# Kernel tuning notes

Measured on AMD Instinct MI355X. Metric: run time of the kernel, lower is better.

Reference implementation:

```python
import jax, jax.numpy as jnp
import numpy as np

N_NODES = 40000
N_EDGES = 320000
N_GRAPHS = 64
IN_DIM = 128
HID4 = 256   # hidden_dim * 4
OUT_DIM = 128
LN_EPS = 1e-5


def setup_inputs() -> dict:
    key = jax.random.key(0)
    ks = jax.random.split(key, 12)
    x = jax.random.normal(ks[0], (N_NODES, IN_DIM), dtype=jnp.float32)
    w = jax.random.uniform(ks[1], (N_EDGES, 4), dtype=jnp.float32)
    src = jax.random.randint(ks[2], (N_EDGES,), 0, N_NODES, dtype=jnp.int32)
    dst = jax.random.randint(ks[3], (N_EDGES,), 0, N_NODES, dtype=jnp.int32)
    graph_ids = jnp.sort(jax.random.randint(ks[4], (N_NODES,), 0, N_GRAPHS, dtype=jnp.int32))
    # parameters (no biases on GraphConv / fc1 linear)
    W1 = jax.random.normal(ks[5], (IN_DIM, HID4), dtype=jnp.float32) / np.sqrt(IN_DIM)
    fc1_W = jax.random.normal(ks[6], (IN_DIM, HID4), dtype=jnp.float32) / np.sqrt(IN_DIM)
    ln_gamma = jnp.ones((HID4,), dtype=jnp.float32)
    ln_beta = jnp.zeros((HID4,), dtype=jnp.float32)
    W2 = jax.random.normal(ks[7], (2 * HID4, HID4), dtype=jnp.float32) / np.sqrt(2 * HID4)
    W3 = jax.random.normal(ks[8], (HID4, OUT_DIM), dtype=jnp.float32) / np.sqrt(HID4)
    return {"x": x, "w": w, "W1": W1, "fc1_W": fc1_W, "ln_gamma": ln_gamma,
            "ln_beta": ln_beta, "W2": W2, "W3": W3,
            "src": src, "dst": dst, "graph_ids": graph_ids}


def _graph_conv(feat, src, dst, ew, W, out_inv_sqrt, in_inv_sqrt):
    # DGL GraphConv, norm='both', bias=False, with scalar edge_weight:
    # h = D_out^{-1/2} x ; m_e = w_e * h[src] ; agg = scatter_add(m, dst) ;
    # out = (D_in^{-1/2} agg) @ W
    h = feat * out_inv_sqrt[:, None]
    m = h[src] * ew[:, None]                       # [E, D] messages
    agg = jax.ops.segment_sum(m, dst, num_segments=N_NODES)
    return (agg * in_inv_sqrt[:, None]) @ W


def reference(x, w, W1, fc1_W, ln_gamma, ln_beta, W2, W3, src, dst, graph_ids):
    # unweighted degree normalization (DGL uses structural degrees, clamp(min=1))
    ones_e = jnp.ones((N_EDGES,), dtype=x.dtype)
    out_deg = jnp.maximum(jax.ops.segment_sum(ones_e, src, num_segments=N_NODES), 1.0)
    in_deg = jnp.maximum(jax.ops.segment_sum(ones_e, dst, num_segments=N_NODES), 1.0)
    out_inv = out_deg ** -0.5
    in_inv = in_deg ** -0.5

    ew = jnp.max(w, axis=1)                        # [E]

    x1 = jax.nn.relu(_graph_conv(x, src, dst, ew, W1, out_inv, in_inv))

    # fc1: Linear(no bias) -> LayerNorm(affine) -> ReLU
    f1 = x @ fc1_W
    mu = jnp.mean(f1, axis=-1, keepdims=True)
    var = jnp.mean((f1 - mu) ** 2, axis=-1, keepdims=True)
    f1 = (f1 - mu) * jax.lax.rsqrt(var + LN_EPS) * ln_gamma + ln_beta
    f1 = jax.nn.relu(f1)

    x1f1 = jnp.concatenate([x1, f1], axis=1)       # [N, 512]
    x2 = jax.nn.relu(_graph_conv(x1f1, src, dst, ew, W2, out_inv, in_inv))
    x3 = jax.nn.relu(_graph_conv(x2, src, dst, ew, W3, out_inv, in_inv))

    # dgl.sum_nodes over batched graph, then row-wise L2 normalize
    readout = jax.ops.segment_sum(x3, graph_ids, num_segments=N_GRAPHS)  # [G, OUT_DIM]
    norm = jnp.maximum(jnp.linalg.norm(readout, axis=1, keepdims=True), 1e-12)
    return readout / norm
```

## Files before the change

kernel.cpp:

```cpp
#include <hip/hip_runtime.h>

#define N_NODES 40000
#define M_PAD   40064
#define N_EDGES 320000
#define N_GRAPHS 64
#define IN_DIM 128
#define HID4 256
#define OUT_DIM 128
#define LN_EPS 1e-5f

typedef short  s16x8  __attribute__((ext_vector_type(8)));
typedef __bf16 bf16x8 __attribute__((ext_vector_type(8)));
typedef float  f32x4  __attribute__((ext_vector_type(4)));

__device__ __forceinline__ unsigned short f2b(float f) {
    unsigned int u = __builtin_bit_cast(unsigned int, f);
    u += 0x7fffu + ((u >> 16) & 1u);
    return (unsigned short)(u >> 16);
}
__device__ __forceinline__ float b2f(unsigned short h) {
    unsigned int u = (unsigned int)h << 16;
    return __builtin_bit_cast(float, u);
}
__device__ __forceinline__ float lo2f(unsigned int u) { return b2f((unsigned short)u); }
__device__ __forceinline__ float hi2f(unsigned int u) { return b2f((unsigned short)(u >> 16)); }
__device__ __forceinline__ unsigned int packb(float x, float y) {
    return (unsigned int)f2b(x) | ((unsigned int)f2b(y) << 16);
}

__device__ __forceinline__ void gll16(const unsigned short* g, short* lds_base) {
    __builtin_amdgcn_global_load_lds(
        (const __attribute__((address_space(1))) unsigned int*)g,
        (__attribute__((address_space(3))) unsigned int*)lds_base, 16, 0, 0);
}


#define XN (N_NODES * IN_DIM)
#define WN 229376
#define PREP_TOT (XN + WN + N_EDGES)

__global__ void prep_all(const float* __restrict__ x, const float* __restrict__ W1,
                         const float* __restrict__ fc1, const float* __restrict__ W2,
                         const float* __restrict__ W3, const float* __restrict__ w,
                         const int* __restrict__ src, const int* __restrict__ dst,
                         unsigned short* __restrict__ xb, unsigned short* __restrict__ W1t,
                         unsigned short* __restrict__ fc1t, unsigned short* __restrict__ W2t,
                         unsigned short* __restrict__ W3t, float* __restrict__ ew,
                         int* __restrict__ cnt_out, int* __restrict__ cnt_in) {
    int idx = blockIdx.x * 256 + threadIdx.x;
    if (idx < XN) { xb[idx] = f2b(x[idx]); return; }
    int j = idx - XN;
    if (j < 32768) { int k = j >> 8, n = j & 255; W1t[n * 128 + k] = f2b(W1[j]); return; }
    j -= 32768;
    if (j < 32768) { int k = j >> 8, n = j & 255; fc1t[n * 128 + k] = f2b(fc1[j]); return; }
    j -= 32768;
    if (j < 131072) { int k = j >> 8, n = j & 255; W2t[n * 512 + k] = f2b(W2[j]); return; }
    j -= 131072;
    if (j < 32768) { int k = j >> 7, n = j & 127; W3t[n * 256 + k] = f2b(W3[j]); return; }
    j -= 32768;
    if (j < N_EDGES) {
        float4 v = ((const float4*)w)[j];
        ew[j] = fmaxf(fmaxf(v.x, v.y), fmaxf(v.z, v.w));
        atomicAdd(&cnt_out[src[j]], 1);
        atomicAdd(&cnt_in[dst[j]], 1);
    }
}

__global__ void scan_part(const int* __restrict__ cnt, int* __restrict__ partial) {
    int b = blockIdx.x;
    int s = 0;
    for (int i = threadIdx.x; i < 1000; i += 256) s += cnt[b * 1000 + i];
#pragma unroll
    for (int m = 1; m < 64; m <<= 1) s += __shfl_xor(s, m);
    __shared__ int wsm[4];
    if ((threadIdx.x & 63) == 0) wsm[threadIdx.x >> 6] = s;
    __syncthreads();
    if (threadIdx.x == 0) partial[b] = wsm[0] + wsm[1] + wsm[2] + wsm[3];
}

__global__ void scan_final(const int* __restrict__ cnt_in, const int* __restrict__ cnt_out,
                           const int* __restrict__ partial, int* __restrict__ off,
                           float* __restrict__ out_inv, float* __restrict__ in_inv) {
    int b = blockIdx.x, tid = threadIdx.x;
    int lane = tid & 63, wv = tid >> 6;
    int pre = 0;
    for (int j = 0; j < b; ++j) pre += partial[j];
    int i = b * 1000 + tid;
    int v = (tid < 1000) ? cnt_in[i] : 0;
    int x = v;
#pragma unroll
    for (int ofs = 1; ofs < 64; ofs <<= 1) {
        int t = __shfl_up(x, ofs);
        if (lane >= ofs) x += t;
    }
    __shared__ int wsum[16];
    if (lane == 63) wsum[wv] = x;
    __syncthreads();
    if (wv == 0 && lane < 16) {
        int s = wsum[lane];
#pragma unroll
        for (int ofs = 1; ofs < 16; ofs <<= 1) {
            int t = __shfl_up(s, ofs);
            if (lane >= ofs) s += t;
        }
        wsum[lane] = s;
    }
    __syncthreads();
    int incl = pre + (wv > 0 ? wsum[wv - 1] : 0) + x;
    if (tid < 1000) {
        off[i] = incl - v;
        in_inv[i] = rsqrtf(fmaxf((float)v, 1.0f));
        out_inv[i] = rsqrtf(fmaxf((float)cnt_out[i], 1.0f));
    }
    if (b == 39 && tid == 999) off[N_NODES] = incl;
}

__global__ void csr_fill(const int* __restrict__ src, const int* __restrict__ dst,
                         const float* __restrict__ ew, const float* __restrict__ out_inv,
                         const int* __restrict__ off, int* __restrict__ cnt_in,
                         int4* __restrict__ es) {
    int e = blockIdx.x * 256 + threadIdx.x;
    if (e >= N_EDGES) return;
    int d = dst[e];
    int slot = off[d] + atomicSub(&cnt_in[d], 1) - 1;
    int s = src[e];
    float wv = ew[e];
    es[slot] = make_int4(s, __float_as_int(wv * out_inv[s]), __float_as_int(wv), 0);
}


template <int D, int RELU, int WSEL>
__global__ void gather_nodes(const unsigned short* __restrict__ h, const int* __restrict__ off,
                             const int4* __restrict__ eg, const float* __restrict__ scale,
                             unsigned short* __restrict__ outb) {
    int n = blockIdx.x;
    int lane = threadIdx.x;
    int b = off[n], e = off[n + 1];
    const uint2* hu = (const uint2*)h;
    float a0 = 0.f, a1 = 0.f, a2 = 0.f, a3 = 0.f;
    if constexpr (D == 256) {
        int i = b;
        for (; i + 3 < e; i += 4) {
            int4 e0 = eg[i], e1 = eg[i + 1], e2 = eg[i + 2], e3 = eg[i + 3];
            uint2 p0 = hu[(size_t)e0.x * 64 + lane];
            uint2 p1 = hu[(size_t)e1.x * 64 + lane];
            uint2 p2 = hu[(size_t)e2.x * 64 + lane];
            uint2 p3 = hu[(size_t)e3.x * 64 + lane];
            float w0 = __int_as_float(WSEL ? e0.z : e0.y);
            float w1 = __int_as_float(WSEL ? e1.z : e1.y);
            float w2 = __int_as_float(WSEL ? e2.z : e2.y);
            float w3 = __int_as_float(WSEL ? e3.z : e3.y);
            a0 += w0 * lo2f(p0.x) + w1 * lo2f(p1.x) + w2 * lo2f(p2.x) + w3 * lo2f(p3.x);
            a1 += w0 * hi2f(p0.x) + w1 * hi2f(p1.x) + w2 * hi2f(p2.x) + w3 * hi2f(p3.x);
            a2 += w0 * lo2f(p0.y) + w1 * lo2f(p1.y) + w2 * lo2f(p2.y) + w3 * lo2f(p3.y);
            a3 += w0 * hi2f(p0.y) + w1 * hi2f(p1.y) + w2 * hi2f(p2.y) + w3 * hi2f(p3.y);
        }
        for (; i < e; ++i) {
            int4 ee = eg[i];
            uint2 p = hu[(size_t)ee.x * 64 + lane];
            float w0 = __int_as_float(WSEL ? ee.z : ee.y);
            a0 += w0 * lo2f(p.x); a1 += w0 * hi2f(p.x);
            a2 += w0 * lo2f(p.y); a3 += w0 * hi2f(p.y);
        }
        float sc = scale[n];
        a0 *= sc; a1 *= sc; a2 *= sc; a3 *= sc;
        if (RELU) {
            a0 = fmaxf(a0, 0.f); a1 = fmaxf(a1, 0.f);
            a2 = fmaxf(a2, 0.f); a3 = fmaxf(a3, 0.f);
        }
        uint2 o; o.x = packb(a0, a1); o.y = packb(a2, a3);
        ((uint2*)outb)[(size_t)n * 64 + lane] = o;
    } else {
        int half = lane >> 5, cl = lane & 31;
        int i = b;
        for (; i + 3 < e; i += 4) {
            int4 ea = eg[i + half];
            int4 eb = eg[i + 2 + half];
            uint2 pa = hu[(size_t)ea.x * 32 + cl];
            uint2 pb = hu[(size_t)eb.x * 32 + cl];
            float wa = __int_as_float(WSEL ? ea.z : ea.y);
            float wb = __int_as_float(WSEL ? eb.z : eb.y);
            a0 += wa * lo2f(pa.x) + wb * lo2f(pb.x);
            a1 += wa * hi2f(pa.x) + wb * hi2f(pb.x);
            a2 += wa * lo2f(pa.y) + wb * lo2f(pb.y);
            a3 += wa * hi2f(pa.y) + wb * hi2f(pb.y);
        }
        for (; i < e; i += 2) {
            int idx = i + half;
            int4 ee = eg[idx < e ? idx : i];
            float w = (idx < e) ? __int_as_float(WSEL ? ee.z : ee.y) : 0.0f;
            uint2 p = hu[(size_t)ee.x * 32 + cl];
            a0 += w * lo2f(p.x); a1 += w * hi2f(p.x);
            a2 += w * lo2f(p.y); a3 += w * hi2f(p.y);
        }
        a0 += __shfl_xor(a0, 32); a1 += __shfl_xor(a1, 32);
        a2 += __shfl_xor(a2, 32); a3 += __shfl_xor(a3, 32);
        float sc = scale[n];
        a0 *= sc; a1 *= sc; a2 *= sc; a3 *= sc;
        if (RELU) {
            a0 = fmaxf(a0, 0.f); a1 = fmaxf(a1, 0.f);
            a2 = fmaxf(a2, 0.f); a3 = fmaxf(a3, 0.f);
        }
        if (half == 0) {
            uint2 o; o.x = packb(a0, a1); o.y = packb(a2, a3);
            ((uint2*)outb)[(size_t)n * 32 + cl] = o;
        }
    }
}


#define G3_NPB 8

__global__ void gather3_ro(const unsigned short* __restrict__ h, const int* __restrict__ off,
                           const int4* __restrict__ eg, const float* __restrict__ scale,
                           const int* __restrict__ gid, float* __restrict__ ro) {
    int lane = threadIdx.x;
    int half = lane >> 5, cl = lane & 31;
    int n0 = blockIdx.x * G3_NPB;
    int n1 = n0 + G3_NPB;
    if (n1 > N_NODES) n1 = N_NODES;
    const uint2* hu = (const uint2*)h;
    float r0 = 0.f, r1 = 0.f, r2 = 0.f, r3 = 0.f;
    int cur = gid[n0];
    for (int n = n0; n < n1; ++n) {
        int g = gid[n];
        if (g != cur) {
            atomicAdd(&ro[cur * OUT_DIM + 4 * cl + 2 * half], half ? r2 : r0);
            atomicAdd(&ro[cur * OUT_DIM + 4 * cl + 2 * half + 1], half ? r3 : r1);
            r0 = r1 = r2 = r3 = 0.f;
            cur = g;
        }
        int b = off[n], e = off[n + 1];
        float a0 = 0.f, a1 = 0.f, a2 = 0.f, a3 = 0.f;
        int i = b;
        for (; i + 3 < e; i += 4) {
            int4 ea = eg[i + half];
            int4 eb = eg[i + 2 + half];
            uint2 pa = hu[(size_t)ea.x * 32 + cl];
            uint2 pb = hu[(size_t)eb.x * 32 + cl];
            float wa = __int_as_float(ea.z), wb = __int_as_float(eb.z);
            a0 += wa * lo2f(pa.x) + wb * lo2f(pb.x);
            a1 += wa * hi2f(pa.x) + wb * hi2f(pb.x);
            a2 += wa * lo2f(pa.y) + wb * lo2f(pb.y);
            a3 += wa * hi2f(pa.y) + wb * hi2f(pb.y);
        }
        for (; i < e; i += 2) {
            int idx = i + half;
            int4 ee = eg[idx < e ? idx : i];
            float w = (idx < e) ? __int_as_float(ee.z) : 0.0f;
            uint2 p = hu[(size_t)ee.x * 32 + cl];
            a0 += w * lo2f(p.x); a1 += w * hi2f(p.x);
            a2 += w * lo2f(p.y); a3 += w * hi2f(p.y);
        }
        a0 += __shfl_xor(a0, 32); a1 += __shfl_xor(a1, 32);
        a2 += __shfl_xor(a2, 32); a3 += __shfl_xor(a3, 32);
        float sc = scale[n];
        r0 += fmaxf(a0 * sc, 0.0f);
        r1 += fmaxf(a1 * sc, 0.0f);
        r2 += fmaxf(a2 * sc, 0.0f);
        r3 += fmaxf(a3 * sc, 0.0f);
    }
    atomicAdd(&ro[cur * OUT_DIM + 4 * cl + 2 * half], half ? r2 : r0);
    atomicAdd(&ro[cur * OUT_DIM + 4 * cl + 2 * half + 1], half ? r3 : r1);
}


__device__ __forceinline__ void gemm_core(short* As, short* Bs,
    const unsigned short* __restrict__ A, const unsigned short* __restrict__ A2,
    const unsigned short* __restrict__ Bt, unsigned short* __restrict__ C,
    const float* __restrict__ rowScaleC, int K1, int K2, int N,
    int relu, int scaleC, int m0, int n0) {
    int tid = threadIdx.x;
    int lane = tid & 63, wave = tid >> 6;
    int wm = (wave >> 1) * 64, wn = (wave & 1) * 64;
    int quad = lane >> 4, r16 = lane & 15;
    const int K = K1 + K2;
    f32x4 acc[4][4] = {};
    int srow = lane >> 3;
    int sk   = ((lane & 7) ^ srow) * 8;
    int xorc = r16 & 7;
    short* ldsA = As + wave * 2048;
    short* ldsB = Bs + wave * 2048;

    for (int k0 = 0; k0 < K; k0 += 64) {
        int kk = k0 + sk;
#pragma unroll
        for (int h = 0; h < 4; ++h) {
            int r = wave * 32 + h * 8 + srow;
            const unsigned short* Ap = (k0 < K1)
                ? A  + (size_t)(m0 + r) * K1 + kk
                : A2 + (size_t)(m0 + r) * K2 + (kk - K1);
            gll16(Ap, ldsA + h * 512);
            gll16(Bt + (size_t)(n0 + r) * K + kk, ldsB + h * 512);
        }
        __syncthreads();
#pragma unroll
        for (int c = 0; c < 2; ++c) {
            s16x8 af[4], bfr[4];
            int pc = (((c * 4 + quad) ^ xorc) << 3);
#pragma unroll
            for (int i = 0; i < 4; ++i)
                af[i] = *(const s16x8*)(As + (wm + i * 16 + r16) * 64 + pc);
#pragma unroll
            for (int j = 0; j < 4; ++j)
                bfr[j] = *(const s16x8*)(Bs + (wn + j * 16 + r16) * 64 + pc);
#pragma unroll
            for (int i = 0; i < 4; ++i)
#pragma unroll
                for (int j = 0; j < 4; ++j)
                    acc[i][j] = __builtin_amdgcn_mfma_f32_16x16x32_bf16(
                        __builtin_bit_cast(bf16x8, af[i]), __builtin_bit_cast(bf16x8, bfr[j]),
                        acc[i][j], 0, 0, 0);
        }
        __syncthreads();
    }

#pragma unroll
    for (int i = 0; i < 4; ++i) {
        int mbase = m0 + wm + i * 16 + quad * 4;
#pragma unroll
        for (int r = 0; r < 4; ++r) {
            int m = mbase + r;
            float sc = scaleC ? rowScaleC[m] : 1.0f;
#pragma unroll
            for (int j = 0; j < 4; ++j) {
                float v = acc[i][j][r] * sc;
                if (relu) v = fmaxf(v, 0.0f);
                C[(size_t)m * N + n0 + wn + j * 16 + r16] = f2b(v);
            }
        }
    }
}

template <int RELU, int SCALE_C>
__global__ __launch_bounds__(256) void gemm_mfma(
    const unsigned short* __restrict__ A, const unsigned short* __restrict__ A2,
    const unsigned short* __restrict__ Bt, unsigned short* __restrict__ C,
    const float* __restrict__ rowScaleC, int K1, int K2, int N) {
    __shared__ short As[8192];
    __shared__ short Bs[8192];
    gemm_core(As, Bs, A, A2, Bt, C, rowScaleC, K1, K2, N, RELU, SCALE_C,
              blockIdx.x * 128, blockIdx.y * 128);
}


__global__ __launch_bounds__(512) void gemm_dual(
    const unsigned short* __restrict__ A0, const unsigned short* __restrict__ B0,
    unsigned short* __restrict__ C0,
    const unsigned short* __restrict__ A1, const unsigned short* __restrict__ B1,
    unsigned short* __restrict__ C1,
    const float* __restrict__ gamma, const float* __restrict__ beta) {
    __shared__ short As[4096];
    __shared__ short Bs[8192];
    __shared__ float lns[128][4];
    __shared__ float lnq[128][4];
    const unsigned short* A  = blockIdx.z ? A1 : A0;
    const unsigned short* Bt = blockIdx.z ? B1 : B0;
    unsigned short* C        = blockIdx.z ? C1 : C0;
    int tid = threadIdx.x;
    int lane = tid & 63, wave = tid >> 6;
    int wm = (wave >> 2) * 64, wn = (wave & 3) * 64;
    int quad = lane >> 4, r16 = lane & 15;
    int m0 = blockIdx.x * 128;
    f32x4 acc[4][4] = {};
    int lrow = lane >> 2;
    int kc = (lane & 3) * 8;
    short* ldsA = As + wave * 512;
    short* ldsB = Bs + wave * 512;

    for (int k0 = 0; k0 < 128; k0 += 32) {
        int kk = k0 + kc;
        int rr = wave * 16 + lrow;
        gll16(A + (size_t)(m0 + rr) * 128 + kk, ldsA);
        gll16(Bt + (size_t)rr * 128 + kk, ldsB);
        gll16(Bt + (size_t)(128 + rr) * 128 + kk, ldsB + 4096);
        __syncthreads();
        s16x8 af[4], bfr[4];
#pragma unroll
        for (int i = 0; i < 4; ++i)
            af[i] = *(const s16x8*)(As + (wm + i * 16 + r16) * 32 + quad * 8);
#pragma unroll
        for (int j = 0; j < 4; ++j)
            bfr[j] = *(const s16x8*)(Bs + (wn + j * 16 + r16) * 32 + quad * 8);
#pragma unroll
        for (int i = 0; i < 4; ++i)
#pragma unroll
            for (int j = 0; j < 4; ++j)
                acc[i][j] = __builtin_amdgcn_mfma_f32_16x16x32_bf16(
                    __builtin_bit_cast(bf16x8, af[i]), __builtin_bit_cast(bf16x8, bfr[j]),
                    acc[i][j], 0, 0, 0);
        __syncthreads();
    }

    if (blockIdx.z == 0) {
#pragma unroll
        for (int i = 0; i < 4; ++i) {
            int mbase = m0 + wm + i * 16 + quad * 4;
#pragma unroll
            for (int r = 0; r < 4; ++r) {
                int m = mbase + r;
#pragma unroll
                for (int j = 0; j < 4; ++j)
                    C[(size_t)m * 256 + wn + j * 16 + r16] = f2b(fmaxf(acc[i][j][r], 0.0f));
            }
        }
    } else {
#pragma unroll
        for (int i = 0; i < 4; ++i)
#pragma unroll
            for (int r = 0; r < 4; ++r) {
                float s = 0.0f, q = 0.0f;
#pragma unroll
                for (int j = 0; j < 4; ++j) { float v = acc[i][j][r]; s += v; q += v * v; }
#pragma unroll
                for (int m = 1; m < 16; m <<= 1) { s += __shfl_xor(s, m); q += __shfl_xor(q, m); }
                if (r16 == 0) {
                    int row = wm + i * 16 + quad * 4 + r;
                    lns[row][wave & 3] = s;
                    lnq[row][wave & 3] = q;
                }
            }
        __syncthreads();
#pragma unroll
        for (int i = 0; i < 4; ++i) {
#pragma unroll
            for (int r = 0; r < 4; ++r) {
                int row = wm + i * 16 + quad * 4 + r;
                float s = lns[row][0] + lns[row][1] + lns[row][2] + lns[row][3];
                float q = lnq[row][0] + lnq[row][1] + lnq[row][2] + lnq[row][3];
                float mu = s * (1.0f / HID4);
                float var = q * (1.0f / HID4) - mu * mu;
                float rs = rsqrtf(var + LN_EPS);
                int m = m0 + row;
#pragma unroll
                for (int j = 0; j < 4; ++j) {
                    int col = wn + j * 16 + r16;
                    float v = (acc[i][j][r] - mu) * rs * gamma[col] + beta[col];
                    C[(size_t)m * 256 + col] = f2b(fmaxf(v, 0.0f));
                }
            }
        }
    }
}


__global__ void normalize_out(const float* __restrict__ ro, float* __restrict__ out) {
    int g = blockIdx.x;
    int d = threadIdx.x;
    float v = ro[g * OUT_DIM + d];
    float ss = v * v;
#pragma unroll
    for (int m = 1; m < 64; m <<= 1) ss += __shfl_xor(ss, m);
    __shared__ float s2[2];
    if ((d & 63) == 0) s2[d >> 6] = ss;
    __syncthreads();
    float tot = s2[0] + s2[1];
    float norm = fmaxf(sqrtf(tot), 1e-12f);
    out[g * OUT_DIM + d] = v / norm;
}


extern "C" void kernel_launch(void* const* d_in, const int* in_sizes, int n_in,
                              void* d_out, int out_size, void* d_ws, size_t ws_size,
                              hipStream_t stream) {
    const float* x    = (const float*)d_in[0];
    const float* w    = (const float*)d_in[1];
    const float* W1   = (const float*)d_in[2];
    const float* fc1W = (const float*)d_in[3];
    const float* gam  = (const float*)d_in[4];
    const float* bet  = (const float*)d_in[5];
    const float* W2   = (const float*)d_in[6];
    const float* W3   = (const float*)d_in[7];
    const int* src = (const int*)d_in[8];
    const int* dst = (const int*)d_in[9];
    const int* gid = (const int*)d_in[10];
    float* out = (float*)d_out;

    float* ws = (float*)d_ws;
    float* out_inv = ws + 0;
    float* in_inv  = ws + 40000;
    float* ew      = ws + 80000;
    int*   cnt_out = (int*)(ws + 400000);
    int*   cnt_in  = (int*)(ws + 440000);
    float* ro      = ws + 480000;
    unsigned short* W1t  = (unsigned short*)(ws + 488192);
    unsigned short* fc1t = (unsigned short*)(ws + 504576);
    unsigned short* W2t  = (unsigned short*)(ws + 520960);
    unsigned short* W3t  = (unsigned short*)(ws + 586496);
    int*   partial = (int*)(ws + 602880);
    int*   off     = (int*)(ws + 602920);
    int4*  es      = (int4*)(ws + 642924);
    unsigned short* xb    = (unsigned short*)(ws + 1923000);
    unsigned short* Q3b   = xb;
    unsigned short* agg1b = (unsigned short*)(ws + 4487100);
    unsigned short* x2b   = agg1b;
    unsigned short* x1b   = (unsigned short*)(ws + 9615300);
    unsigned short* f1b   = (unsigned short*)(ws + 14743500);
    unsigned short* P2b   = (unsigned short*)(ws + 19871700);

    hipMemsetAsync(cnt_out, 0, (2 * 40000 + N_GRAPHS * OUT_DIM) * sizeof(float), stream);

    prep_all<<<(PREP_TOT + 255) / 256, 256, 0, stream>>>(x, W1, fc1W, W2, W3, w, src, dst,
                                                         xb, W1t, fc1t, W2t, W3t, ew,
                                                         cnt_out, cnt_in);
    scan_part<<<40, 256, 0, stream>>>(cnt_in, partial);
    scan_final<<<40, 1024, 0, stream>>>(cnt_in, cnt_out, partial, off, out_inv, in_inv);
    csr_fill<<<(N_EDGES + 255) / 256, 256, 0, stream>>>(src, dst, ew, out_inv, off, cnt_in, es);

    gather_nodes<IN_DIM, 0, 0><<<N_NODES, 64, 0, stream>>>(xb, off, es, in_inv, agg1b);
    {
        dim3 grid(M_PAD / 128, 1, 2);
        gemm_dual<<<grid, 512, 0, stream>>>(agg1b, W1t, x1b, xb, fc1t, f1b, gam, bet);
    }

    {
        dim3 grid(M_PAD / 128, HID4 / 128);
        gemm_mfma<0, 1><<<grid, 256, 0, stream>>>(x1b, f1b, W2t, P2b, out_inv,
                                                  HID4, HID4, HID4);
    }
    gather_nodes<HID4, 1, 1><<<N_NODES, 64, 0, stream>>>(P2b, off, es, in_inv, x2b);

    {
        dim3 grid(M_PAD / 128, OUT_DIM / 128);
        gemm_mfma<0, 1><<<grid, 256, 0, stream>>>(x2b, nullptr, W3t, Q3b, out_inv,
                                                  HID4, 0, OUT_DIM);
    }
    gather3_ro<<<(N_NODES + G3_NPB - 1) / G3_NPB, 64, 0, stream>>>(Q3b, off, es, in_inv,
                                                                   gid, ro);
    normalize_out<<<N_GRAPHS, 128, 0, stream>>>(ro, out);
}
```

Measured before the change: 285.0 us.

## Vectorize gathers and conversion, pack waves per block, fuse CSR fill with fc1 GEMM

The x-to-bf16 conversion now handles 8 elements per thread with float4 loads and uint4 stores. The gather kernels load 16-byte rows per lane and run 8 nodes per 512-thread block (one wave per node) instead of one 64-thread block per node. The CSR fill is merged into one launch with the fc1+LayerNorm GEMM, so the two independent jobs can overlap. The first graph-conv GEMM becomes its own kernel. The aim is wider memory transactions, fewer tiny blocks and more concurrency, at the cost of more padding lanes on low-degree nodes and a mixed-role kernel whose shared-memory footprint also applies to its edge blocks.

```diff
diff --git a/kernel.cpp b/kernel.cpp
--- a/kernel.cpp
+++ b/kernel.cpp
@@ -36,8 +36,9 @@
 
 
 #define XN (N_NODES * IN_DIM)
+#define XT (XN / 8)
 #define WN 229376
-#define PREP_TOT (XN + WN + N_EDGES)
+#define PREP_TOT (XT + WN + N_EDGES)
 
 __global__ void prep_all(const float* __restrict__ x, const float* __restrict__ W1,
                          const float* __restrict__ fc1, const float* __restrict__ W2,
@@ -48,8 +49,16 @@
                          unsigned short* __restrict__ W3t, float* __restrict__ ew,
                          int* __restrict__ cnt_out, int* __restrict__ cnt_in) {
     int idx = blockIdx.x * 256 + threadIdx.x;
-    if (idx < XN) { xb[idx] = f2b(x[idx]); return; }
-    int j = idx - XN;
+    if (idx < XT) {
+        const float4* xv = (const float4*)x;
+        float4 u = xv[idx * 2], v = xv[idx * 2 + 1];
+        uint4 o;
+        o.x = packb(u.x, u.y); o.y = packb(u.z, u.w);
+        o.z = packb(v.x, v.y); o.w = packb(v.z, v.w);
+        ((uint4*)xb)[idx] = o;
+        return;
+    }
+    int j = idx - XT;
     if (j < 32768) { int k = j >> 8, n = j & 255; W1t[n * 128 + k] = f2b(W1[j]); return; }
     j -= 32768;
     if (j < 32768) { int k = j >> 8, n = j & 255; fc1t[n * 128 + k] = f2b(fc1[j]); return; }
@@ -115,153 +124,263 @@
     if (b == 39 && tid == 999) off[N_NODES] = incl;
 }
 
-__global__ void csr_fill(const int* __restrict__ src, const int* __restrict__ dst,
-                         const float* __restrict__ ew, const float* __restrict__ out_inv,
-                         const int* __restrict__ off, int* __restrict__ cnt_in,
-                         int4* __restrict__ es) {
-    int e = blockIdx.x * 256 + threadIdx.x;
-    if (e >= N_EDGES) return;
-    int d = dst[e];
-    int slot = off[d] + atomicSub(&cnt_in[d], 1) - 1;
-    int s = src[e];
-    float wv = ew[e];
-    es[slot] = make_int4(s, __float_as_int(wv * out_inv[s]), __float_as_int(wv), 0);
-}
-
+
+__global__ __launch_bounds__(512) void csr_fc1(
+    const int* __restrict__ src, const int* __restrict__ dst,
+    const float* __restrict__ ew, const float* __restrict__ out_inv,
+    const int* __restrict__ off, int* __restrict__ cnt_in, int4* __restrict__ es,
+    const unsigned short* __restrict__ A, const unsigned short* __restrict__ Bt,
+    unsigned short* __restrict__ C,
+    const float* __restrict__ gamma, const float* __restrict__ beta) {
+    __shared__ short As[4096];
+    __shared__ short Bs[8192];
+    __shared__ float lns[128][4];
+    __shared__ float lnq[128][4];
+    if (blockIdx.x < 625) {
+        int e = blockIdx.x * 512 + threadIdx.x;
+        if (e >= N_EDGES) return;
+        int d = dst[e];
+        int slot = off[d] + atomicSub(&cnt_in[d], 1) - 1;
+        int s = src[e];
+        float wv = ew[e];
+        es[slot] = make_int4(s, __float_as_int(wv * out_inv[s]), __float_as_int(wv), 0);
+        return;
+    }
+    int m0 = (blockIdx.x - 625) * 128;
+    int tid = threadIdx.x;
+    int lane = tid & 63, wave = tid >> 6;
+    int wm = (wave >> 2) * 64, wn = (wave & 3) * 64;
+    int quad = lane >> 4, r16 = lane & 15;
+    f32x4 acc[4][4] = {};
+    int lrow = lane >> 2;
+    int kc = (lane & 3) * 8;
+    short* ldsA = As + wave * 512;
+    short* ldsB = Bs + wave * 512;
+
+    for (int k0 = 0; k0 < 128; k0 += 32) {
+        int kk = k0 + kc;
+        int rr = wave * 16 + lrow;
+        gll16(A + (size_t)(m0 + rr) * 128 + kk, ldsA);
+        gll16(Bt + (size_t)rr * 128 + kk, ldsB);
+        gll16(Bt + (size_t)(128 + rr) * 128 + kk, ldsB + 4096);
+        __syncthreads();
+        s16x8 af[4], bfr[4];
+#pragma unroll
+        for (int i = 0; i < 4; ++i)
+            af[i] = *(const s16x8*)(As + (wm + i * 16 + r16) * 32 + quad * 8);
+#pragma unroll
+        for (int j = 0; j < 4; ++j)
+            bfr[j] = *(const s16x8*)(Bs + (wn + j * 16 + r16) * 32 + quad * 8);
+#pragma unroll
+        for (int i = 0; i < 4; ++i)
+#pragma unroll
+            for (int j = 0; j < 4; ++j)
+                acc[i][j] = __builtin_amdgcn_mfma_f32_16x16x32_bf16(
+                    __builtin_bit_cast(bf16x8, af[i]), __builtin_bit_cast(bf16x8, bfr[j]),
+                    acc[i][j], 0, 0, 0);
+        __syncthreads();
+    }
+
+#pragma unroll
+    for (int i = 0; i < 4; ++i)
+#pragma unroll
+        for (int r = 0; r < 4; ++r) {
+            float s = 0.0f, q = 0.0f;
+#pragma unroll
+            for (int j = 0; j < 4; ++j) { float v = acc[i][j][r]; s += v; q += v * v; }
+#pragma unroll
+            for (int m = 1; m < 16; m <<= 1) { s += __shfl_xor(s, m); q += __shfl_xor(q, m); }
+            if (r16 == 0) {
+                int row = wm + i * 16 + quad * 4 + r;
+                lns[row][wave & 3] = s;
+                lnq[row][wave & 3] = q;
+            }
+        }
+    __syncthreads();
+#pragma unroll
+    for (int i = 0; i < 4; ++i) {
+#pragma unroll
+        for (int r = 0; r < 4; ++r) {
+            int row = wm + i * 16 + quad * 4 + r;
+            float s = lns[row][0] + lns[row][1] + lns[row][2] + lns[row][3];
+            float q = lnq[row][0] + lnq[row][1] + lnq[row][2] + lnq[row][3];
+            float mu = s * (1.0f / HID4);
+            float var = q * (1.0f / HID4) - mu * mu;
+            float rs = rsqrtf(var + LN_EPS);
+            int m = m0 + row;
+#pragma unroll
+            for (int j = 0; j < 4; ++j) {
+                int col = wn + j * 16 + r16;
+                float v = (acc[i][j][r] - mu) * rs * gamma[col] + beta[col];
+                C[(size_t)m * 256 + col] = f2b(fmaxf(v, 0.0f));
+            }
+        }
+    }
+}
+
+
+template <int RELU, int WSEL>
+__device__ __forceinline__ void gather_wave_128(int n, int lane,
+        const unsigned short* __restrict__ h, const int* __restrict__ off,
+        const int4* __restrict__ eg, const float* __restrict__ scale,
+        unsigned short* __restrict__ outb) {
+    int b = off[n], e = off[n + 1];
+    int quad = lane >> 4, ql = lane & 15;
+    const uint4* hu = (const uint4*)h;
+    float a0 = 0.f, a1 = 0.f, a2 = 0.f, a3 = 0.f, a4 = 0.f, a5 = 0.f, a6 = 0.f, a7 = 0.f;
+    for (int i = b; i < e; i += 4) {
+        int idx = i + quad;
+        int4 ee = eg[idx < e ? idx : b];
+        float w = (idx < e) ? __int_as_float(WSEL ? ee.z : ee.y) : 0.0f;
+        uint4 p = hu[(size_t)ee.x * 16 + ql];
+        a0 += w * lo2f(p.x); a1 += w * hi2f(p.x);
+        a2 += w * lo2f(p.y); a3 += w * hi2f(p.y);
+        a4 += w * lo2f(p.z); a5 += w * hi2f(p.z);
+        a6 += w * lo2f(p.w); a7 += w * hi2f(p.w);
+    }
+    a0 += __shfl_xor(a0, 16); a1 += __shfl_xor(a1, 16);
+    a2 += __shfl_xor(a2, 16); a3 += __shfl_xor(a3, 16);
+    a4 += __shfl_xor(a4, 16); a5 += __shfl_xor(a5, 16);
+    a6 += __shfl_xor(a6, 16); a7 += __shfl_xor(a7, 16);
+    a0 += __shfl_xor(a0, 32); a1 += __shfl_xor(a1, 32);
+    a2 += __shfl_xor(a2, 32); a3 += __shfl_xor(a3, 32);
+    a4 += __shfl_xor(a4, 32); a5 += __shfl_xor(a5, 32);
+    a6 += __shfl_xor(a6, 32); a7 += __shfl_xor(a7, 32);
+    float sc = scale[n];
+    a0 *= sc; a1 *= sc; a2 *= sc; a3 *= sc; a4 *= sc; a5 *= sc; a6 *= sc; a7 *= sc;
+    if (RELU) {
+        a0 = fmaxf(a0, 0.f); a1 = fmaxf(a1, 0.f); a2 = fmaxf(a2, 0.f); a3 = fmaxf(a3, 0.f);
+        a4 = fmaxf(a4, 0.f); a5 = fmaxf(a5, 0.f); a6 = fmaxf(a6, 0.f); a7 = fmaxf(a7, 0.f);
+    }
+    if (quad == 0) {
+        uint4 o;
+        o.x = packb(a0, a1); o.y = packb(a2, a3); o.z = packb(a4, a5); o.w = packb(a6, a7);
+        ((uint4*)outb)[(size_t)n * 16 + ql] = o;
+    }
+}
+
+template <int RELU, int WSEL>
+__device__ __forceinline__ void gather_wave_256(int n, int lane,
+        const unsigned short* __restrict__ h, const int* __restrict__ off,
+        const int4* __restrict__ eg, const float* __restrict__ scale,
+        unsigned short* __restrict__ outb) {
+    int b = off[n], e = off[n + 1];
+    int half = lane >> 5, cl = lane & 31;
+    const uint4* hu = (const uint4*)h;
+    float a0 = 0.f, a1 = 0.f, a2 = 0.f, a3 = 0.f, a4 = 0.f, a5 = 0.f, a6 = 0.f, a7 = 0.f;
+    int i = b;
+    for (; i + 3 < e; i += 4) {
+        int4 ea = eg[i + half], eb = eg[i + 2 + half];
+        uint4 pa = hu[(size_t)ea.x * 32 + cl];
+        uint4 pb = hu[(size_t)eb.x * 32 + cl];
+        float wa = __int_as_float(WSEL ? ea.z : ea.y);
+        float wb = __int_as_float(WSEL ? eb.z : eb.y);
+        a0 += wa * lo2f(pa.x) + wb * lo2f(pb.x); a1 += wa * hi2f(pa.x) + wb * hi2f(pb.x);
+        a2 += wa * lo2f(pa.y) + wb * lo2f(pb.y); a3 += wa * hi2f(pa.y) + wb * hi2f(pb.y);
+        a4 += wa * lo2f(pa.z) + wb * lo2f(pb.z); a5 += wa * hi2f(pa.z) + wb * hi2f(pb.z);
+        a6 += wa * lo2f(pa.w) + wb * lo2f(pb.w); a7 += wa * hi2f(pa.w) + wb * hi2f(pb.w);
+    }
+    for (; i < e; i += 2) {
+        int idx = i + half;
+        int4 ee = eg[idx < e ? idx : b];
+        float w = (idx < e) ? __int_as_float(WSEL ? ee.z : ee.y) : 0.0f;
+        uint4 p = hu[(size_t)ee.x * 32 + cl];
+        a0 += w * lo2f(p.x); a1 += w * hi2f(p.x);
+        a2 += w * lo2f(p.y); a3 += w * hi2f(p.y);
+        a4 += w * lo2f(p.z); a5 += w * hi2f(p.z);
+        a6 += w * lo2f(p.w); a7 += w * hi2f(p.w);
+    }
+    a0 += __shfl_xor(a0, 32); a1 += __shfl_xor(a1, 32);
+    a2 += __shfl_xor(a2, 32); a3 += __shfl_xor(a3, 32);
+    a4 += __shfl_xor(a4, 32); a5 += __shfl_xor(a5, 32);
+    a6 += __shfl_xor(a6, 32); a7 += __shfl_xor(a7, 32);
+    float sc = scale[n];
+    a0 *= sc; a1 *= sc; a2 *= sc; a3 *= sc; a4 *= sc; a5 *= sc; a6 *= sc; a7 *= sc;
+    if (RELU) {
+        a0 = fmaxf(a0, 0.f); a1 = fmaxf(a1, 0.f); a2 = fmaxf(a2, 0.f); a3 = fmaxf(a3, 0.f);
+        a4 = fmaxf(a4, 0.f); a5 = fmaxf(a5, 0.f); a6 = fmaxf(a6, 0.f); a7 = fmaxf(a7, 0.f);
+    }
+    if (half == 0) {
+        uint4 o;
+        o.x = packb(a0, a1); o.y = packb(a2, a3); o.z = packb(a4, a5); o.w = packb(a6, a7);
+        ((uint4*)outb)[(size_t)n * 32 + cl] = o;
+    }
+}
 
 template <int D, int RELU, int WSEL>
-__global__ void gather_nodes(const unsigned short* __restrict__ h, const int* __restrict__ off,
-                             const int4* __restrict__ eg, const float* __restrict__ scale,
-                             unsigned short* __restrict__ outb) {
-    int n = blockIdx.x;
-    int lane = threadIdx.x;
-    int b = off[n], e = off[n + 1];
-    const uint2* hu = (const uint2*)h;
-    float a0 = 0.f, a1 = 0.f, a2 = 0.f, a3 = 0.f;
-    if constexpr (D == 256) {
-        int i = b;
-        for (; i + 3 < e; i += 4) {
-            int4 e0 = eg[i], e1 = eg[i + 1], e2 = eg[i + 2], e3 = eg[i + 3];
-            uint2 p0 = hu[(size_t)e0.x * 64 + lane];
-            uint2 p1 = hu[(size_t)e1.x * 64 + lane];
-            uint2 p2 = hu[(size_t)e2.x * 64 + lane];
-            uint2 p3 = hu[(size_t)e3.x * 64 + lane];
-            float w0 = __int_as_float(WSEL ? e0.z : e0.y);
-            float w1 = __int_as_float(WSEL ? e1.z : e1.y);
-            float w2 = __int_as_float(WSEL ? e2.z : e2.y);
-            float w3 = __int_as_float(WSEL ? e3.z : e3.y);
-            a0 += w0 * lo2f(p0.x) + w1 * lo2f(p1.x) + w2 * lo2f(p2.x) + w3 * lo2f(p3.x);
-            a1 += w0 * hi2f(p0.x) + w1 * hi2f(p1.x) + w2 * hi2f(p2.x) + w3 * hi2f(p3.x);
-            a2 += w0 * lo2f(p0.y) + w1 * lo2f(p1.y) + w2 * lo2f(p2.y) + w3 * lo2f(p3.y);
-            a3 += w0 * hi2f(p0.y) + w1 * hi2f(p1.y) + w2 * hi2f(p2.y) + w3 * hi2f(p3.y);
-        }
-        for (; i < e; ++i) {
-            int4 ee = eg[i];
-            uint2 p = hu[(size_t)ee.x * 64 + lane];
-            float w0 = __int_as_float(WSEL ? ee.z : ee.y);
-            a0 += w0 * lo2f(p.x); a1 += w0 * hi2f(p.x);
-            a2 += w0 * lo2f(p.y); a3 += w0 * hi2f(p.y);
-        }
-        float sc = scale[n];
-        a0 *= sc; a1 *= sc; a2 *= sc; a3 *= sc;
-        if (RELU) {
-            a0 = fmaxf(a0, 0.f); a1 = fmaxf(a1, 0.f);
-            a2 = fmaxf(a2, 0.f); a3 = fmaxf(a3, 0.f);
-        }
-        uint2 o; o.x = packb(a0, a1); o.y = packb(a2, a3);
-        ((uint2*)outb)[(size_t)n * 64 + lane] = o;
-    } else {
-        int half = lane >> 5, cl = lane & 31;
-        int i = b;
-        for (; i + 3 < e; i += 4) {
-            int4 ea = eg[i + half];
-            int4 eb = eg[i + 2 + half];
-            uint2 pa = hu[(size_t)ea.x * 32 + cl];
-            uint2 pb = hu[(size_t)eb.x * 32 + cl];
-            float wa = __int_as_float(WSEL ? ea.z : ea.y);
-            float wb = __int_as_float(WSEL ? eb.z : eb.y);
-            a0 += wa * lo2f(pa.x) + wb * lo2f(pb.x);
-            a1 += wa * hi2f(pa.x) + wb * hi2f(pb.x);
-            a2 += wa * lo2f(pa.y) + wb * lo2f(pb.y);
-            a3 += wa * hi2f(pa.y) + wb * hi2f(pb.y);
-        }
-        for (; i < e; i += 2) {
-            int idx = i + half;
-            int4 ee = eg[idx < e ? idx : i];
-            float w = (idx < e) ? __int_as_float(WSEL ? ee.z : ee.y) : 0.0f;
-            uint2 p = hu[(size_t)ee.x * 32 + cl];
-            a0 += w * lo2f(p.x); a1 += w * hi2f(p.x);
-            a2 += w * lo2f(p.y); a3 += w * hi2f(p.y);
-        }
-        a0 += __shfl_xor(a0, 32); a1 += __shfl_xor(a1, 32);
-        a2 += __shfl_xor(a2, 32); a3 += __shfl_xor(a3, 32);
-        float sc = scale[n];
-        a0 *= sc; a1 *= sc; a2 *= sc; a3 *= sc;
-        if (RELU) {
-            a0 = fmaxf(a0, 0.f); a1 = fmaxf(a1, 0.f);
-            a2 = fmaxf(a2, 0.f); a3 = fmaxf(a3, 0.f);
-        }
-        if (half == 0) {
-            uint2 o; o.x = packb(a0, a1); o.y = packb(a2, a3);
-            ((uint2*)outb)[(size_t)n * 32 + cl] = o;
-        }
-    }
+__global__ __launch_bounds__(512) void gather_nodes(
+        const unsigned short* __restrict__ h, const int* __restrict__ off,
+        const int4* __restrict__ eg, const float* __restrict__ scale,
+        unsigned short* __restrict__ outb) {
+    int wave = threadIdx.x >> 6, lane = threadIdx.x & 63;
+    int n = blockIdx.x * 8 + wave;
+    if (n >= N_NODES) return;
+    if constexpr (D == 256)
+        gather_wave_256<RELU, WSEL>(n, lane, h, off, eg, scale, outb);
+    else
+        gather_wave_128<RELU, WSEL>(n, lane, h, off, eg, scale, outb);
 }
 
 
 #define G3_NPB 8
 
-__global__ void gather3_ro(const unsigned short* __restrict__ h, const int* __restrict__ off,
-                           const int4* __restrict__ eg, const float* __restrict__ scale,
-                           const int* __restrict__ gid, float* __restrict__ ro) {
-    int lane = threadIdx.x;
-    int half = lane >> 5, cl = lane & 31;
-    int n0 = blockIdx.x * G3_NPB;
+__global__ __launch_bounds__(512) void gather3_ro(
+        const unsigned short* __restrict__ h, const int* __restrict__ off,
+        const int4* __restrict__ eg, const float* __restrict__ scale,
+        const int* __restrict__ gid, float* __restrict__ ro) {
+    int wave = threadIdx.x >> 6, lane = threadIdx.x & 63;
+    int quad = lane >> 4, ql = lane & 15;
+    int n0 = (blockIdx.x * 8 + wave) * G3_NPB;
+    if (n0 >= N_NODES) return;
     int n1 = n0 + G3_NPB;
     if (n1 > N_NODES) n1 = N_NODES;
-    const uint2* hu = (const uint2*)h;
-    float r0 = 0.f, r1 = 0.f, r2 = 0.f, r3 = 0.f;
+    const uint4* hu = (const uint4*)h;
+    float r0 = 0.f, r1 = 0.f, r2 = 0.f, r3 = 0.f, r4 = 0.f, r5 = 0.f, r6 = 0.f, r7 = 0.f;
     int cur = gid[n0];
     for (int n = n0; n < n1; ++n) {
         int g = gid[n];
         if (g != cur) {
-            atomicAdd(&ro[cur * OUT_DIM + 4 * cl + 2 * half], half ? r2 : r0);
-            atomicAdd(&ro[cur * OUT_DIM + 4 * cl + 2 * half + 1], half ? r3 : r1);
-            r0 = r1 = r2 = r3 = 0.f;
+            if (quad == 0) {
+                float* p = &ro[cur * OUT_DIM + ql * 8];
+                atomicAdd(p + 0, r0); atomicAdd(p + 1, r1); atomicAdd(p + 2, r2);
+                atomicAdd(p + 3, r3); atomicAdd(p + 4, r4); atomicAdd(p + 5, r5);
+                atomicAdd(p + 6, r6); atomicAdd(p + 7, r7);
+            }
+            r0 = r1 = r2 = r3 = r4 = r5 = r6 = r7 = 0.f;
             cur = g;
         }
         int b = off[n], e = off[n + 1];
-        float a0 = 0.f, a1 = 0.f, a2 = 0.f, a3 = 0.f;
-        int i = b;
-        for (; i + 3 < e; i += 4) {
-            int4 ea = eg[i + half];
-            int4 eb = eg[i + 2 + half];
-            uint2 pa = hu[(size_t)ea.x * 32 + cl];
-            uint2 pb = hu[(size_t)eb.x * 32 + cl];
-            float wa = __int_as_float(ea.z), wb = __int_as_float(eb.z);
-            a0 += wa * lo2f(pa.x) + wb * lo2f(pb.x);
-            a1 += wa * hi2f(pa.x) + wb * hi2f(pb.x);
-            a2 += wa * lo2f(pa.y) + wb * lo2f(pb.y);
-            a3 += wa * hi2f(pa.y) + wb * hi2f(pb.y);
-        }
-        for (; i < e; i += 2) {
-            int idx = i + half;
-            int4 ee = eg[idx < e ? idx : i];
+        float a0 = 0.f, a1 = 0.f, a2 = 0.f, a3 = 0.f, a4 = 0.f, a5 = 0.f, a6 = 0.f, a7 = 0.f;
+        for (int i = b; i < e; i += 4) {
+            int idx = i + quad;
+            int4 ee = eg[idx < e ? idx : b];
             float w = (idx < e) ? __int_as_float(ee.z) : 0.0f;
-            uint2 p = hu[(size_t)ee.x * 32 + cl];
+            uint4 p = hu[(size_t)ee.x * 16 + ql];
             a0 += w * lo2f(p.x); a1 += w * hi2f(p.x);
             a2 += w * lo2f(p.y); a3 += w * hi2f(p.y);
-        }
+            a4 += w * lo2f(p.z); a5 += w * hi2f(p.z);
+            a6 += w * lo2f(p.w); a7 += w * hi2f(p.w);
+        }
+        a0 += __shfl_xor(a0, 16); a1 += __shfl_xor(a1, 16);
+        a2 += __shfl_xor(a2, 16); a3 += __shfl_xor(a3, 16);
+        a4 += __shfl_xor(a4, 16); a5 += __shfl_xor(a5, 16);
+        a6 += __shfl_xor(a6, 16); a7 += __shfl_xor(a7, 16);
         a0 += __shfl_xor(a0, 32); a1 += __shfl_xor(a1, 32);
         a2 += __shfl_xor(a2, 32); a3 += __shfl_xor(a3, 32);
+        a4 += __shfl_xor(a4, 32); a5 += __shfl_xor(a5, 32);
+        a6 += __shfl_xor(a6, 32); a7 += __shfl_xor(a7, 32);
         float sc = scale[n];
-        r0 += fmaxf(a0 * sc, 0.0f);
-        r1 += fmaxf(a1 * sc, 0.0f);
-        r2 += fmaxf(a2 * sc, 0.0f);
-        r3 += fmaxf(a3 * sc, 0.0f);
-    }
-    atomicAdd(&ro[cur * OUT_DIM + 4 * cl + 2 * half], half ? r2 : r0);
-    atomicAdd(&ro[cur * OUT_DIM + 4 * cl + 2 * half + 1], half ? r3 : r1);
+        r0 += fmaxf(a0 * sc, 0.0f); r1 += fmaxf(a1 * sc, 0.0f);
+        r2 += fmaxf(a2 * sc, 0.0f); r3 += fmaxf(a3 * sc, 0.0f);
+        r4 += fmaxf(a4 * sc, 0.0f); r5 += fmaxf(a5 * sc, 0.0f);
+        r6 += fmaxf(a6 * sc, 0.0f); r7 += fmaxf(a7 * sc, 0.0f);
+    }
+    if (quad == 0) {
+        float* p = &ro[cur * OUT_DIM + ql * 8];
+        atomicAdd(p + 0, r0); atomicAdd(p + 1, r1); atomicAdd(p + 2, r2);
+        atomicAdd(p + 3, r3); atomicAdd(p + 4, r4); atomicAdd(p + 5, r5);
+        atomicAdd(p + 6, r6); atomicAdd(p + 7, r7);
+    }
 }
 
 
@@ -344,19 +463,11 @@
 }
 
 
-__global__ __launch_bounds__(512) void gemm_dual(
-    const unsigned short* __restrict__ A0, const unsigned short* __restrict__ B0,
-    unsigned short* __restrict__ C0,
-    const unsigned short* __restrict__ A1, const unsigned short* __restrict__ B1,
-    unsigned short* __restrict__ C1,
-    const float* __restrict__ gamma, const float* __restrict__ beta) {
+__global__ __launch_bounds__(512) void gemm_conv1(
+    const unsigned short* __restrict__ A, const unsigned short* __restrict__ Bt,
+    unsigned short* __restrict__ C) {
     __shared__ short As[4096];
     __shared__ short Bs[8192];
-    __shared__ float lns[128][4];
-    __shared__ float lnq[128][4];
-    const unsigned short* A  = blockIdx.z ? A1 : A0;
-    const unsigned short* Bt = blockIdx.z ? B1 : B0;
-    unsigned short* C        = blockIdx.z ? C1 : C0;
     int tid = threadIdx.x;
     int lane = tid & 63, wave = tid >> 6;
     int wm = (wave >> 2) * 64, wn = (wave & 3) * 64;
@@ -392,53 +503,15 @@
         __syncthreads();
     }
 
-    if (blockIdx.z == 0) {
-#pragma unroll
-        for (int i = 0; i < 4; ++i) {
-            int mbase = m0 + wm + i * 16 + quad * 4;
-#pragma unroll
-            for (int r = 0; r < 4; ++r) {
-                int m = mbase + r;
-#pragma unroll
-                for (int j = 0; j < 4; ++j)
-                    C[(size_t)m * 256 + wn + j * 16 + r16] = f2b(fmaxf(acc[i][j][r], 0.0f));
-            }
-        }
-    } else {
-#pragma unroll
-        for (int i = 0; i < 4; ++i)
-#pragma unroll
-            for (int r = 0; r < 4; ++r) {
-                float s = 0.0f, q = 0.0f;
-#pragma unroll
-                for (int j = 0; j < 4; ++j) { float v = acc[i][j][r]; s += v; q += v * v; }
-#pragma unroll
-                for (int m = 1; m < 16; m <<= 1) { s += __shfl_xor(s, m); q += __shfl_xor(q, m); }
-                if (r16 == 0) {
-                    int row = wm + i * 16 + quad * 4 + r;
-                    lns[row][wave & 3] = s;
-                    lnq[row][wave & 3] = q;
-                }
-            }
-        __syncthreads();
-#pragma unroll
-        for (int i = 0; i < 4; ++i) {
-#pragma unroll
-            for (int r = 0; r < 4; ++r) {
-                int row = wm + i * 16 + quad * 4 + r;
-                float s = lns[row][0] + lns[row][1] + lns[row][2] + lns[row][3];
-                float q = lnq[row][0] + lnq[row][1] + lnq[row][2] + lnq[row][3];
-                float mu = s * (1.0f / HID4);
-                float var = q * (1.0f / HID4) - mu * mu;
-                float rs = rsqrtf(var + LN_EPS);
-                int m = m0 + row;
-#pragma unroll
-                for (int j = 0; j < 4; ++j) {
-                    int col = wn + j * 16 + r16;
-                    float v = (acc[i][j][r] - mu) * rs * gamma[col] + beta[col];
-                    C[(size_t)m * 256 + col] = f2b(fmaxf(v, 0.0f));
-                }
-            }
+#pragma unroll
+    for (int i = 0; i < 4; ++i) {
+        int mbase = m0 + wm + i * 16 + quad * 4;
+#pragma unroll
+        for (int r = 0; r < 4; ++r) {
+            int m = mbase + r;
+#pragma unroll
+            for (int j = 0; j < 4; ++j)
+                C[(size_t)m * 256 + wn + j * 16 + r16] = f2b(fmaxf(acc[i][j][r], 0.0f));
         }
     }
 }
@@ -505,27 +578,25 @@
                                                          cnt_out, cnt_in);
     scan_part<<<40, 256, 0, stream>>>(cnt_in, partial);
     scan_final<<<40, 1024, 0, stream>>>(cnt_in, cnt_out, partial, off, out_inv, in_inv);
-    csr_fill<<<(N_EDGES + 255) / 256, 256, 0, stream>>>(src, dst, ew, out_inv, off, cnt_in, es);
-
-    gather_nodes<IN_DIM, 0, 0><<<N_NODES, 64, 0, stream>>>(xb, off, es, in_inv, agg1b);
-    {
-        dim3 grid(M_PAD / 128, 1, 2);
-        gemm_dual<<<grid, 512, 0, stream>>>(agg1b, W1t, x1b, xb, fc1t, f1b, gam, bet);
-    }
+
+    csr_fc1<<<625 + 313, 512, 0, stream>>>(src, dst, ew, out_inv, off, cnt_in, es,
+                                           xb, fc1t, f1b, gam, bet);
+
+    gather_nodes<IN_DIM, 0, 0><<<5000, 512, 0, stream>>>(xb, off, es, in_inv, agg1b);
+    gemm_conv1<<<313, 512, 0, stream>>>(agg1b, W1t, x1b);
 
     {
         dim3 grid(M_PAD / 128, HID4 / 128);
         gemm_mfma<0, 1><<<grid, 256, 0, stream>>>(x1b, f1b, W2t, P2b, out_inv,
                                                   HID4, HID4, HID4);
     }
-    gather_nodes<HID4, 1, 1><<<N_NODES, 64, 0, stream>>>(P2b, off, es, in_inv, x2b);
+    gather_nodes<HID4, 1, 1><<<5000, 512, 0, stream>>>(P2b, off, es, in_inv, x2b);
 
     {
         dim3 grid(M_PAD / 128, OUT_DIM / 128);
         gemm_mfma<0, 1><<<grid, 256, 0, stream>>>(x2b, nullptr, W3t, Q3b, out_inv,
                                                   HID4, 0, OUT_DIM);
     }
-    gather3_ro<<<(N_NODES + G3_NPB - 1) / G3_NPB, 64, 0, stream>>>(Q3b, off, es, in_inv,
-                                                                   gid, ro);
+    gather3_ro<<<625, 512, 0, stream>>>(Q3b, off, es, in_inv, gid, ro);
     normalize_out<<<N_GRAPHS, 128, 0, stream>>>(ro, out);
 }
```

Result: slower. 313.0 us (+9.8%).
